# Optimization experiments

Hardware: AMD Instinct MI355X
Metric: run time of the kernel (lower is better)

Reference implementation:

```python
import jax, jax.numpy as jnp
import numpy as np

S, L, B = 64, 64, 16
D_IN, D_ATTN = 1024, 512


def setup_inputs() -> dict:
    key = jax.random.key(0)
    ks = jax.random.split(key, 8)
    context = jax.random.normal(ks[0], (S, L, B, D_IN), dtype=jnp.float32)
    query = jax.random.normal(ks[1], (L, B, D_IN), dtype=jnp.float32)
    mask = jnp.ones((S, L, B), dtype=jnp.int32)
    # Linear params (torch layout: weight [out, in], bias [out])
    sc = 1.0 / np.sqrt(D_IN)
    Wc = jax.random.uniform(ks[2], (D_ATTN, D_IN), minval=-sc, maxval=sc, dtype=jnp.float32)
    bc = jax.random.uniform(ks[3], (D_ATTN,), minval=-sc, maxval=sc, dtype=jnp.float32)
    Wq = jax.random.uniform(ks[4], (D_ATTN, D_IN), minval=-sc, maxval=sc, dtype=jnp.float32)
    bq = jax.random.uniform(ks[5], (D_ATTN,), minval=-sc, maxval=sc, dtype=jnp.float32)
    v = jax.random.uniform(ks[6], (D_ATTN,), dtype=jnp.float32)  # torch.rand -> U[0,1)
    return {"context": context, "query": query, "mask": mask,
            "Wc": Wc, "bc": bc, "Wq": Wq, "bq": bq, "v": v}


def reference(context, query, mask, Wc, bc, Wq, bq, v):
    # context: [s,l,b,din], query: [l,b,din]
    context_proj = jnp.einsum('slbi,di->slbd', context, Wc) + bc  # [s,l,b,da]
    query_proj = jnp.einsum('lbi,di->lbd', query, Wq) + bq        # [l,b,da]
    scores = jnp.tanh(context_proj + query_proj[None])            # [s,l,b,da]
    scores = jnp.einsum('slbd,d->slb', scores, v)                 # [s,l,b]
    scores = jnp.where(mask == 0, jnp.float32(-1e9), scores)
    alpha = jax.nn.softmax(scores, axis=0)                        # softmax over s
    attn_output = jnp.einsum('slb,slbd->lbd', alpha, context)     # [l,b,din]
    return (attn_output, alpha)
```

## Files before the change

kernel.cpp:

```cpp
#include <hip/hip_runtime.h>
#include <hip/hip_fp16.h>
#include <stdint.h>

#define S_DIM 64
#define L_DIM 64
#define B_DIM 16
#define LB    1024
#define DIN   1024
#define DA    512
#define M_TOT 65536

#define BM 64
#define BN 256
#define BK 64
#define NT (DIN / BK)

using f16x8 = __attribute__((ext_vector_type(8))) _Float16;
using f32x4 = __attribute__((ext_vector_type(4))) float;

typedef const __attribute__((address_space(1))) void* gas_ptr;
typedef __attribute__((address_space(3))) void* las_ptr;

__device__ __forceinline__ void load_lds16(const void* g, void* l) {
    __builtin_amdgcn_global_load_lds((gas_ptr)g, (las_ptr)l, 16, 0, 0);
}

__device__ __forceinline__ float fast_tanh(float x) {
    return 1.0f - 2.0f / (__expf(2.0f * x) + 1.0f);
}

__global__ void cvt_all(const float* __restrict__ Wc, const float* __restrict__ Wq,
                        const float* __restrict__ q,
                        _Float16* __restrict__ Wch, _Float16* __restrict__ Wqh,
                        _Float16* __restrict__ Qh) {
    int i = blockIdx.x * 256 + threadIdx.x;
    if (i < DA * DIN)            Wch[i] = (_Float16)Wc[i];
    else if (i < 2 * DA * DIN)   Wqh[i - DA * DIN] = (_Float16)Wq[i - DA * DIN];
    else                         Qh[i - 2 * DA * DIN] = (_Float16)q[i - 2 * DA * DIN];
}

__global__ __launch_bounds__(256) void qp_gemm(
    const _Float16* __restrict__ Qh,
    const _Float16* __restrict__ Wqh,
    const float* __restrict__ bq, const float* __restrict__ bc,
    float* __restrict__ qp)
{
    __shared__ __align__(16) _Float16 lA[64 * 64];
    __shared__ __align__(16) _Float16 lB[64 * 64];
    const int t = threadIdx.x;
    const int w = t >> 6, lane = t & 63;
    const int quad = lane >> 4, m16 = lane & 15;
    const int n0 = blockIdx.x * 64, lb0 = blockIdx.y * 64;

    f32x4 acc[4] = {};

    for (int kt = 0; kt < DIN / 64; ++kt) {
#pragma unroll
        for (int i = 0; i < 2; ++i) {
            int c = (w * 2 + i) * 64 + lane;
            int row = c >> 3;
            int kc = (c & 7) ^ (row & 7);
            load_lds16(Qh  + (size_t)(lb0 + row) * DIN + kt * 64 + kc * 8, (char*)lA + (size_t)c * 16);
            load_lds16(Wqh + (size_t)(n0  + row) * DIN + kt * 64 + kc * 8, (char*)lB + (size_t)c * 16);
        }
        __syncthreads();
#pragma unroll
        for (int kk = 0; kk < 64; kk += 32) {
            int cq = (kk >> 3) + quad;
            int ar = 16 * w + m16;
            f16x8 a = *(const f16x8*)((const char*)lA + ar * 128 + ((cq ^ (ar & 7)) * 16));
#pragma unroll
            for (int j = 0; j < 4; ++j) {
                int br = 16 * j + m16;
                f16x8 b = *(const f16x8*)((const char*)lB + br * 128 + ((cq ^ (br & 7)) * 16));
                acc[j] = __builtin_amdgcn_mfma_f32_16x16x32_f16(a, b, acc[j], 0, 0, 0);
            }
        }
        __syncthreads();
    }
#pragma unroll
    for (int j = 0; j < 4; ++j) {
        int n = n0 + 16 * j + m16;
        float bias = bq[n] + bc[n];
#pragma unroll
        for (int r = 0; r < 4; ++r) {
            int lb = lb0 + 16 * w + quad * 4 + r;
            qp[(size_t)lb * DA + n] = acc[j][r] + bias;
        }
    }
}

__global__ __launch_bounds__(256, 3) void score_gemm6(
    const float* __restrict__ ctx,
    const _Float16* __restrict__ Wch,
    const float* __restrict__ qp,
    const float* __restrict__ v,
    _Float16* __restrict__ ctxh,
    float* __restrict__ sc)
{
    __shared__ __align__(16) _Float16 lA[BM * BK];
    __shared__ __align__(16) _Float16 lB[BN * BK];
    __shared__ float lP[4][BM];

    const int t = threadIdx.x;
    const int w = t >> 6, lane = t & 63;
    const int quad = lane >> 4, m16 = lane & 15;
    const int wn = w;

    int bid = blockIdx.x;
    int xcd = bid & 7;
    int idx = bid >> 3;
    const int nq = idx & 1;
    const int mb = xcd * 128 + (idx >> 1);
    const int m0 = mb * BM;
    const int n0 = nq * BN;
    const int lb0 = m0 & (LB - 1);
    const bool wr_ctxh = (nq == 0);

    const int arow = t >> 2;
    const int c0   = (t & 3) * 2;

    auto stageB = [&](int kt) {
#pragma unroll
        for (int i = 0; i < 8; ++i) {
            int c = (w * 8 + i) * 64 + lane;
            int row = c >> 3;
            int kc = (c & 7) ^ (row & 7);
            load_lds16(Wch + (size_t)(n0 + row) * DIN + kt * BK + kc * 8,
                       (char*)lB + (size_t)c * 16);
        }
    };

    f32x4 pf[4];
    auto issueA = [&](int kt) {
        const float* p = ctx + (size_t)(m0 + arow) * DIN + kt * BK + c0 * 8;
        pf[0] = *(const f32x4*)(p);
        pf[1] = *(const f32x4*)(p + 4);
        pf[2] = *(const f32x4*)(p + 8);
        pf[3] = *(const f32x4*)(p + 12);
    };

    issueA(0);

    f32x4 acc[4][4];
#pragma unroll
    for (int i = 0; i < 4; ++i) {
        int rl = lb0 + 16 * i + quad * 4;
#pragma unroll
        for (int j = 0; j < 4; ++j) {
            int n = n0 + wn * 64 + 16 * j + m16;
#pragma unroll
            for (int r = 0; r < 4; ++r)
                acc[i][j][r] = qp[(size_t)(rl + r) * DA + n];
        }
    }

    for (int kt = 0; kt < NT; ++kt) {
        stageB(kt);

        f16x8 h0 = {(_Float16)pf[0][0], (_Float16)pf[0][1], (_Float16)pf[0][2], (_Float16)pf[0][3],
                    (_Float16)pf[1][0], (_Float16)pf[1][1], (_Float16)pf[1][2], (_Float16)pf[1][3]};
        f16x8 h1 = {(_Float16)pf[2][0], (_Float16)pf[2][1], (_Float16)pf[2][2], (_Float16)pf[2][3],
                    (_Float16)pf[3][0], (_Float16)pf[3][1], (_Float16)pf[3][2], (_Float16)pf[3][3]};
        *(f16x8*)((char*)lA + arow * 128 + (((c0)     ^ (arow & 7)) * 16)) = h0;
        *(f16x8*)((char*)lA + arow * 128 + (((c0 + 1) ^ (arow & 7)) * 16)) = h1;
        if (wr_ctxh) {
            _Float16* cd = ctxh + (size_t)(m0 + arow) * DIN + kt * BK + c0 * 8;
            *(f16x8*)cd = h0;
            *(f16x8*)(cd + 8) = h1;
        }

        issueA(kt + 1 < NT ? kt + 1 : NT - 1);

        if (wr_ctxh) asm volatile("s_waitcnt vmcnt(6)" ::: "memory");
        else         asm volatile("s_waitcnt vmcnt(4)" ::: "memory");
        asm volatile("s_waitcnt lgkmcnt(0)" ::: "memory");
        __builtin_amdgcn_s_barrier();
        __builtin_amdgcn_sched_barrier(0);

#pragma unroll
        for (int kk2 = 0; kk2 < 2; ++kk2) {
            int cq = kk2 * 4 + quad;
            f16x8 a[4], b[4];
#pragma unroll
            for (int i = 0; i < 4; ++i) {
                int ar = 16 * i + m16;
                a[i] = *(const f16x8*)((const char*)lA + ar * 128 + ((cq ^ (ar & 7)) * 16));
            }
#pragma unroll
            for (int j = 0; j < 4; ++j) {
                int br = wn * 64 + 16 * j + m16;
                b[j] = *(const f16x8*)((const char*)lB + br * 128 + ((cq ^ (br & 7)) * 16));
            }
            __builtin_amdgcn_s_setprio(1);
#pragma unroll
            for (int i = 0; i < 4; ++i)
#pragma unroll
                for (int j = 0; j < 4; ++j)
                    acc[i][j] = __builtin_amdgcn_mfma_f32_16x16x32_f16(a[i], b[j], acc[i][j], 0, 0, 0);
            __builtin_amdgcn_s_setprio(0);
        }

        __builtin_amdgcn_sched_barrier(0);
        __builtin_amdgcn_s_barrier();
        __builtin_amdgcn_sched_barrier(0);
    }

    float vv[4];
#pragma unroll
    for (int j = 0; j < 4; ++j) vv[j] = v[n0 + wn * 64 + 16 * j + m16];

    float part[16];
#pragma unroll
    for (int i = 0; i < 4; ++i)
#pragma unroll
        for (int r = 0; r < 4; ++r) {
            float s = 0.f;
#pragma unroll
            for (int j = 0; j < 4; ++j)
                s += fast_tanh(acc[i][j][r]) * vv[j];
            part[i * 4 + r] = s;
        }
#pragma unroll
    for (int off = 1; off < 16; off <<= 1) {
#pragma unroll
        for (int k = 0; k < 16; ++k) part[k] += __shfl_xor(part[k], off, 64);
    }
    if (m16 == 0) {
#pragma unroll
        for (int k = 0; k < 16; ++k) {
            int rl = 16 * (k >> 2) + quad * 4 + (k & 3);
            lP[wn][rl] = part[k];
        }
    }
    __syncthreads();
    if (t < BM) {
        float s = lP[0][t] + lP[1][t] + lP[2][t] + lP[3][t];
        sc[(size_t)nq * M_TOT + m0 + t] = s;
    }
}

__global__ __launch_bounds__(256, 3) void score_gemm(
    const float* __restrict__ ctx, const _Float16* __restrict__ Wch,
    const float* __restrict__ qp, const float* __restrict__ v,
    float* __restrict__ scores)
{
    __shared__ __align__(16) _Float16 lA[128 * 64];
    __shared__ __align__(16) _Float16 lB[128 * 64];
    __shared__ float lP[2][128];

    const int t = threadIdx.x;
    const int w = t >> 6, lane = t & 63;
    const int quad = lane >> 4, m16 = lane & 15;
    const int wm = w & 1, wn = w >> 1;

    int bid = blockIdx.x;
    int xcd = bid & 7;
    int j2 = bid >> 3;
    int nqf = j2 & 3;
    int mbf = ((j2 >> 2) << 3) | xcd;
    const int m0 = mbf * 128;
    const int n0 = nqf * 128;

    f32x4 acc[4][4] = {};

    const int arow = t >> 1;
    const int akc4 = (t & 1) * 4;
    const float* gA = ctx + (size_t)(m0 + arow) * DIN + (t & 1) * 32;

    for (int kt = 0; kt < DIN / 64; ++kt) {
        {
            const float* p = gA + kt * 64;
            f32x4 f[8];
#pragma unroll
            for (int qd = 0; qd < 8; ++qd) f[qd] = *(const f32x4*)(p + qd * 4);
#pragma unroll
            for (int q2 = 0; q2 < 4; ++q2) {
                f16x8 h = {(_Float16)f[2*q2][0], (_Float16)f[2*q2][1],
                           (_Float16)f[2*q2][2], (_Float16)f[2*q2][3],
                           (_Float16)f[2*q2+1][0], (_Float16)f[2*q2+1][1],
                           (_Float16)f[2*q2+1][2], (_Float16)f[2*q2+1][3]};
                int c = akc4 + q2;
                *(f16x8*)((char*)lA + arow * 128 + ((c ^ (arow & 7)) * 16)) = h;
            }
        }
#pragma unroll
        for (int i = 0; i < 4; ++i) {
            int c = (w * 4 + i) * 64 + lane;
            int row = c >> 3;
            int kc = (c & 7) ^ (row & 7);
            load_lds16(Wch + (size_t)(n0 + row) * DIN + kt * 64 + kc * 8, (char*)lB + (size_t)c * 16);
        }
        __syncthreads();
#pragma unroll
        for (int kk = 0; kk < 64; kk += 32) {
            int cq = (kk >> 3) + quad;
            f16x8 a[4], b[4];
#pragma unroll
            for (int i = 0; i < 4; ++i) {
                int ar = wm * 64 + 16 * i + m16;
                a[i] = *(const f16x8*)((const char*)lA + ar * 128 + ((cq ^ (ar & 7)) * 16));
            }
#pragma unroll
            for (int j = 0; j < 4; ++j) {
                int br = wn * 64 + 16 * j + m16;
                b[j] = *(const f16x8*)((const char*)lB + br * 128 + ((cq ^ (br & 7)) * 16));
            }
#pragma unroll
            for (int i = 0; i < 4; ++i)
#pragma unroll
                for (int j = 0; j < 4; ++j)
                    acc[i][j] = __builtin_amdgcn_mfma_f32_16x16x32_f16(a[i], b[j], acc[i][j], 0, 0, 0);
        }
        __syncthreads();
    }

    float vv[4];
    int nn[4];
#pragma unroll
    for (int j = 0; j < 4; ++j) { nn[j] = n0 + wn * 64 + 16 * j + m16; vv[j] = v[nn[j]]; }

    float part[16];
#pragma unroll
    for (int i = 0; i < 4; ++i) {
#pragma unroll
        for (int r = 0; r < 4; ++r) {
            int gm = m0 + wm * 64 + 16 * i + quad * 4 + r;
            int lb = gm & (LB - 1);
            float s = 0.f;
#pragma unroll
            for (int j = 0; j < 4; ++j) {
                float x = acc[i][j][r] + qp[(size_t)lb * DA + nn[j]];
                s += fast_tanh(x) * vv[j];
            }
            part[i * 4 + r] = s;
        }
    }
#pragma unroll
    for (int off = 1; off < 16; off <<= 1) {
#pragma unroll
        for (int k = 0; k < 16; ++k) part[k] += __shfl_xor(part[k], off, 64);
    }
    if (m16 == 0) {
#pragma unroll
        for (int k = 0; k < 16; ++k) {
            int row_local = wm * 64 + 16 * (k >> 2) + quad * 4 + (k & 3);
            lP[wn][row_local] = part[k];
        }
    }
    __syncthreads();
    if (t < 128) {
        float s = lP[0][t] + lP[1][t];
        atomicAdd(&scores[m0 + t], s);
    }
}

__global__ __launch_bounds__(64) void softmax3(const float* __restrict__ sc,
                                               const int* __restrict__ mask,
                                               float* __restrict__ alpha) {
    int lb = blockIdx.x;
    int s = threadIdx.x;
    int m = s * LB + lb;
    float x = sc[m] + sc[M_TOT + m];
    if (mask[m] == 0) x = -1e9f;
    float mx = x;
#pragma unroll
    for (int off = 1; off < 64; off <<= 1) mx = fmaxf(mx, __shfl_xor(mx, off, 64));
    float e = __expf(x - mx);
    float sum = e;
#pragma unroll
    for (int off = 1; off < 64; off <<= 1) sum += __shfl_xor(sum, off, 64);
    alpha[m] = e / sum;
}

__global__ __launch_bounds__(64) void softmax2(const float* __restrict__ scores,
                                               const int* __restrict__ mask,
                                               float* __restrict__ alpha) {
    int lb = blockIdx.x;
    int s = threadIdx.x;
    float x = scores[s * LB + lb];
    if (mask[s * LB + lb] == 0) x = -1e9f;
    float mx = x;
#pragma unroll
    for (int off = 1; off < 64; off <<= 1) mx = fmaxf(mx, __shfl_xor(mx, off, 64));
    float e = __expf(x - mx);
    float sum = e;
#pragma unroll
    for (int off = 1; off < 64; off <<= 1) sum += __shfl_xor(sum, off, 64);
    alpha[s * LB + lb] = e / sum;
}

__global__ __launch_bounds__(128) void weighted_sum2(
    const _Float16* __restrict__ ctxh, const float* __restrict__ alpha,
    float* __restrict__ out) {
    __shared__ float lAl[S_DIM];
    const int lb = blockIdx.x;
    const int t = threadIdx.x;
    if (t < S_DIM) lAl[t] = alpha[t * LB + lb];
    __syncthreads();
    float acc[8] = {};
    const _Float16* base = ctxh + (size_t)lb * DIN + t * 8;
#pragma unroll 8
    for (int s = 0; s < S_DIM; ++s) {
        float a = lAl[s];
        f16x8 c = *(const f16x8*)(base + (size_t)s * LB * DIN);
#pragma unroll
        for (int j = 0; j < 8; ++j) acc[j] += a * (float)c[j];
    }
    f32x4 lo = {acc[0], acc[1], acc[2], acc[3]};
    f32x4 hi = {acc[4], acc[5], acc[6], acc[7]};
    *(f32x4*)(out + (size_t)lb * DIN + t * 8) = lo;
    *(f32x4*)(out + (size_t)lb * DIN + t * 8 + 4) = hi;
}

__global__ __launch_bounds__(256) void weighted_sum(
    const float* __restrict__ ctx, const float* __restrict__ alpha,
    float* __restrict__ out) {
    __shared__ float lAl[S_DIM];
    const int lb = blockIdx.x;
    const int t = threadIdx.x;
    if (t < S_DIM) lAl[t] = alpha[t * LB + lb];
    __syncthreads();
    f32x4 acc = {0.f, 0.f, 0.f, 0.f};
    const float* base = ctx + (size_t)lb * DIN + t * 4;
#pragma unroll 4
    for (int s = 0; s < S_DIM; ++s) {
        float a = lAl[s];
        f32x4 c = *(const f32x4*)(base + (size_t)s * LB * DIN);
        acc += a * c;
    }
    *(f32x4*)(out + (size_t)lb * DIN + t * 4) = acc;
}

extern "C" void kernel_launch(void* const* d_in, const int* in_sizes, int n_in,
                              void* d_out, int out_size, void* d_ws, size_t ws_size,
                              hipStream_t stream) {
    (void)in_sizes; (void)n_in; (void)out_size;
    const float* ctx   = (const float*)d_in[0];
    const float* query = (const float*)d_in[1];
    const int*   mask  = (const int*)d_in[2];
    const float* Wc    = (const float*)d_in[3];
    const float* bc    = (const float*)d_in[4];
    const float* Wq    = (const float*)d_in[5];
    const float* bq    = (const float*)d_in[6];
    const float* v     = (const float*)d_in[7];

    float* out_attn  = (float*)d_out;
    float* out_alpha = (float*)d_out + (size_t)LB * DIN;

    char* ws = (char*)d_ws;
    _Float16* Wch = (_Float16*)(ws);
    _Float16* Wqh = (_Float16*)(ws + (1 << 20));
    _Float16* Qh  = (_Float16*)(ws + (2 << 20));
    float*    qp  = (float*)(ws + (4 << 20));
    float*    sc  = (float*)(ws + (6 << 20));
    _Float16* ctxh = (_Float16*)(ws + (8 << 20));

    const size_t need = (size_t)(8 + 128) << 20;
    const bool bigws = ws_size >= need;

    cvt_all<<<(2 * DA * DIN + LB * DIN) / 256, 256, 0, stream>>>(Wc, Wq, query, Wch, Wqh, Qh);
    qp_gemm<<<dim3(DA / 64, LB / 64), 256, 0, stream>>>(Qh, Wqh, bq, bc, qp);

    if (bigws) {
        score_gemm6<<<(M_TOT / BM) * (DA / BN), 256, 0, stream>>>(ctx, Wch, qp, v, ctxh, sc);
        softmax3<<<LB, 64, 0, stream>>>(sc, mask, out_alpha);
        weighted_sum2<<<LB, 128, 0, stream>>>(ctxh, out_alpha, out_attn);
    } else {
        hipMemsetAsync(sc, 0, (size_t)M_TOT * sizeof(float), stream);
        score_gemm<<<2048, 256, 0, stream>>>(ctx, Wch, qp, v, sc);
        softmax2<<<LB, 64, 0, stream>>>(sc, mask, out_alpha);
        weighted_sum<<<LB, 256, 0, stream>>>(ctx, out_alpha, out_attn);
    }
}
```

Measured before the change: 496.7 us.

## Double-buffer score GEMM LDS, halve N tile, split weighted sum over s

The score GEMM now uses double-buffered LDS for the A and B tiles. The next k-tile is converted and staged while the current one feeds the MFMAs, and the trailing barrier per iteration is gone. The N tile shrinks from 256 to 128, so four blocks per M tile each write partial scores, and softmax now sums four partial score planes. The weighted sum kernel uses 512 threads, splitting the s loop four ways and reducing through shared memory to raise parallelism. The trade-off is that context is re-read and converted by four blocks per M tile instead of two, adding global traffic.

```diff
diff --git a/kernel.cpp b/kernel.cpp
--- a/kernel.cpp
+++ b/kernel.cpp
@@ -11,7 +11,7 @@
 #define M_TOT 65536
 
 #define BM 64
-#define BN 256
+#define BN 128
 #define BK 64
 #define NT (DIN / BK)
 
@@ -90,7 +90,7 @@
     }
 }
 
-__global__ __launch_bounds__(256, 3) void score_gemm6(
+__global__ __launch_bounds__(256, 3) void score_gemm7(
     const float* __restrict__ ctx,
     const _Float16* __restrict__ Wch,
     const float* __restrict__ qp,
@@ -98,8 +98,8 @@
     _Float16* __restrict__ ctxh,
     float* __restrict__ sc)
 {
-    __shared__ __align__(16) _Float16 lA[BM * BK];
-    __shared__ __align__(16) _Float16 lB[BN * BK];
+    __shared__ __align__(16) _Float16 lA[2][BM * BK];
+    __shared__ __align__(16) _Float16 lB[2][BN * BK];
     __shared__ float lP[4][BM];
 
     const int t = threadIdx.x;
@@ -110,8 +110,8 @@
     int bid = blockIdx.x;
     int xcd = bid & 7;
     int idx = bid >> 3;
-    const int nq = idx & 1;
-    const int mb = xcd * 128 + (idx >> 1);
+    const int nq = idx & 3;
+    const int mb = xcd * 128 + (idx >> 2);
     const int m0 = mb * BM;
     const int n0 = nq * BN;
     const int lb0 = m0 & (LB - 1);
@@ -120,14 +120,14 @@
     const int arow = t >> 2;
     const int c0   = (t & 3) * 2;
 
-    auto stageB = [&](int kt) {
-#pragma unroll
-        for (int i = 0; i < 8; ++i) {
-            int c = (w * 8 + i) * 64 + lane;
+    auto stageB = [&](int kt, int buf) {
+#pragma unroll
+        for (int i = 0; i < 4; ++i) {
+            int c = (w * 4 + i) * 64 + lane;
             int row = c >> 3;
             int kc = (c & 7) ^ (row & 7);
             load_lds16(Wch + (size_t)(n0 + row) * DIN + kt * BK + kc * 8,
-                       (char*)lB + (size_t)c * 16);
+                       (char*)lB[buf] + (size_t)c * 16);
         }
     };
 
@@ -140,75 +140,83 @@
         pf[3] = *(const f32x4*)(p + 12);
     };
 
-    issueA(0);
-
-    f32x4 acc[4][4];
-#pragma unroll
-    for (int i = 0; i < 4; ++i) {
-        int rl = lb0 + 16 * i + quad * 4;
-#pragma unroll
-        for (int j = 0; j < 4; ++j) {
-            int n = n0 + wn * 64 + 16 * j + m16;
-#pragma unroll
-            for (int r = 0; r < 4; ++r)
-                acc[i][j][r] = qp[(size_t)(rl + r) * DA + n];
-        }
-    }
-
-    for (int kt = 0; kt < NT; ++kt) {
-        stageB(kt);
-
+    auto cvtStore = [&](int kts) {
         f16x8 h0 = {(_Float16)pf[0][0], (_Float16)pf[0][1], (_Float16)pf[0][2], (_Float16)pf[0][3],
                     (_Float16)pf[1][0], (_Float16)pf[1][1], (_Float16)pf[1][2], (_Float16)pf[1][3]};
         f16x8 h1 = {(_Float16)pf[2][0], (_Float16)pf[2][1], (_Float16)pf[2][2], (_Float16)pf[2][3],
                     (_Float16)pf[3][0], (_Float16)pf[3][1], (_Float16)pf[3][2], (_Float16)pf[3][3]};
-        *(f16x8*)((char*)lA + arow * 128 + (((c0)     ^ (arow & 7)) * 16)) = h0;
-        *(f16x8*)((char*)lA + arow * 128 + (((c0 + 1) ^ (arow & 7)) * 16)) = h1;
+        char* base = (char*)lA[kts & 1];
+        *(f16x8*)(base + arow * 128 + (((c0)     ^ (arow & 7)) * 16)) = h0;
+        *(f16x8*)(base + arow * 128 + (((c0 + 1) ^ (arow & 7)) * 16)) = h1;
         if (wr_ctxh) {
-            _Float16* cd = ctxh + (size_t)(m0 + arow) * DIN + kt * BK + c0 * 8;
+            _Float16* cd = ctxh + (size_t)(m0 + arow) * DIN + kts * BK + c0 * 8;
             *(f16x8*)cd = h0;
             *(f16x8*)(cd + 8) = h1;
         }
-
-        issueA(kt + 1 < NT ? kt + 1 : NT - 1);
-
-        if (wr_ctxh) asm volatile("s_waitcnt vmcnt(6)" ::: "memory");
-        else         asm volatile("s_waitcnt vmcnt(4)" ::: "memory");
+    };
+
+    issueA(0);
+
+    f32x4 acc[4][2];
+#pragma unroll
+    for (int i = 0; i < 4; ++i) {
+        int rl = lb0 + 16 * i + quad * 4;
+#pragma unroll
+        for (int j = 0; j < 2; ++j) {
+            int n = n0 + wn * 32 + 16 * j + m16;
+#pragma unroll
+            for (int r = 0; r < 4; ++r)
+                acc[i][j][r] = qp[(size_t)(rl + r) * DA + n];
+        }
+    }
+
+    cvtStore(0);
+    stageB(0, 0);
+    issueA(1);
+
+    for (int kt = 0; kt < NT; ++kt) {
+        const int cur = kt & 1;
+
+        if (kt == NT - 1) asm volatile("s_waitcnt vmcnt(0)" ::: "memory");
+        else              asm volatile("s_waitcnt vmcnt(4)" ::: "memory");
         asm volatile("s_waitcnt lgkmcnt(0)" ::: "memory");
         __builtin_amdgcn_s_barrier();
         __builtin_amdgcn_sched_barrier(0);
 
+        if (kt + 1 < NT) {
+            cvtStore(kt + 1);
+            stageB(kt + 1, cur ^ 1);
+            if (kt + 2 < NT) issueA(kt + 2);
+        }
+        __builtin_amdgcn_sched_barrier(0);
+
 #pragma unroll
         for (int kk2 = 0; kk2 < 2; ++kk2) {
             int cq = kk2 * 4 + quad;
-            f16x8 a[4], b[4];
+            f16x8 a[4], b[2];
 #pragma unroll
             for (int i = 0; i < 4; ++i) {
                 int ar = 16 * i + m16;
-                a[i] = *(const f16x8*)((const char*)lA + ar * 128 + ((cq ^ (ar & 7)) * 16));
-            }
-#pragma unroll
-            for (int j = 0; j < 4; ++j) {
-                int br = wn * 64 + 16 * j + m16;
-                b[j] = *(const f16x8*)((const char*)lB + br * 128 + ((cq ^ (br & 7)) * 16));
+                a[i] = *(const f16x8*)((const char*)lA[cur] + ar * 128 + ((cq ^ (ar & 7)) * 16));
+            }
+#pragma unroll
+            for (int j = 0; j < 2; ++j) {
+                int br = wn * 32 + 16 * j + m16;
+                b[j] = *(const f16x8*)((const char*)lB[cur] + br * 128 + ((cq ^ (br & 7)) * 16));
             }
             __builtin_amdgcn_s_setprio(1);
 #pragma unroll
             for (int i = 0; i < 4; ++i)
 #pragma unroll
-                for (int j = 0; j < 4; ++j)
+                for (int j = 0; j < 2; ++j)
                     acc[i][j] = __builtin_amdgcn_mfma_f32_16x16x32_f16(a[i], b[j], acc[i][j], 0, 0, 0);
             __builtin_amdgcn_s_setprio(0);
         }
-
-        __builtin_amdgcn_sched_barrier(0);
-        __builtin_amdgcn_s_barrier();
-        __builtin_amdgcn_sched_barrier(0);
-    }
-
-    float vv[4];
-#pragma unroll
-    for (int j = 0; j < 4; ++j) vv[j] = v[n0 + wn * 64 + 16 * j + m16];
+    }
+
+    float vv[2];
+#pragma unroll
+    for (int j = 0; j < 2; ++j) vv[j] = v[n0 + wn * 32 + 16 * j + m16];
 
     float part[16];
 #pragma unroll
@@ -217,7 +225,7 @@
         for (int r = 0; r < 4; ++r) {
             float s = 0.f;
 #pragma unroll
-            for (int j = 0; j < 4; ++j)
+            for (int j = 0; j < 2; ++j)
                 s += fast_tanh(acc[i][j][r]) * vv[j];
             part[i * 4 + r] = s;
         }
@@ -355,13 +363,13 @@
     }
 }
 
-__global__ __launch_bounds__(64) void softmax3(const float* __restrict__ sc,
+__global__ __launch_bounds__(64) void softmax4(const float* __restrict__ sc,
                                                const int* __restrict__ mask,
                                                float* __restrict__ alpha) {
     int lb = blockIdx.x;
     int s = threadIdx.x;
     int m = s * LB + lb;
-    float x = sc[m] + sc[M_TOT + m];
+    float x = sc[m] + sc[M_TOT + m] + sc[2 * M_TOT + m] + sc[3 * M_TOT + m];
     if (mask[m] == 0) x = -1e9f;
     float mx = x;
 #pragma unroll
@@ -390,27 +398,41 @@
     alpha[s * LB + lb] = e / sum;
 }
 
-__global__ __launch_bounds__(128) void weighted_sum2(
+__global__ __launch_bounds__(512) void weighted_sum3(
     const _Float16* __restrict__ ctxh, const float* __restrict__ alpha,
     float* __restrict__ out) {
     __shared__ float lAl[S_DIM];
+    __shared__ float red[4][DIN];
     const int lb = blockIdx.x;
     const int t = threadIdx.x;
     if (t < S_DIM) lAl[t] = alpha[t * LB + lb];
     __syncthreads();
+    const int d8 = t & 127;
+    const int sq = t >> 7;
     float acc[8] = {};
-    const _Float16* base = ctxh + (size_t)lb * DIN + t * 8;
-#pragma unroll 8
-    for (int s = 0; s < S_DIM; ++s) {
+    const _Float16* base = ctxh + (size_t)lb * DIN + d8 * 8;
+#pragma unroll 4
+    for (int s = sq * 16; s < sq * 16 + 16; ++s) {
         float a = lAl[s];
         f16x8 c = *(const f16x8*)(base + (size_t)s * LB * DIN);
 #pragma unroll
         for (int j = 0; j < 8; ++j) acc[j] += a * (float)c[j];
     }
-    f32x4 lo = {acc[0], acc[1], acc[2], acc[3]};
-    f32x4 hi = {acc[4], acc[5], acc[6], acc[7]};
-    *(f32x4*)(out + (size_t)lb * DIN + t * 8) = lo;
-    *(f32x4*)(out + (size_t)lb * DIN + t * 8 + 4) = hi;
+#pragma unroll
+    for (int j = 0; j < 8; ++j) red[sq][d8 * 8 + j] = acc[j];
+    __syncthreads();
+    if (t < 128) {
+        float o[8];
+#pragma unroll
+        for (int j = 0; j < 8; ++j) {
+            int d = t * 8 + j;
+            o[j] = red[0][d] + red[1][d] + red[2][d] + red[3][d];
+        }
+        f32x4 lo = {o[0], o[1], o[2], o[3]};
+        f32x4 hi = {o[4], o[5], o[6], o[7]};
+        *(f32x4*)(out + (size_t)lb * DIN + t * 8) = lo;
+        *(f32x4*)(out + (size_t)lb * DIN + t * 8 + 4) = hi;
+    }
 }
 
 __global__ __launch_bounds__(256) void weighted_sum(
@@ -463,9 +485,9 @@
     qp_gemm<<<dim3(DA / 64, LB / 64), 256, 0, stream>>>(Qh, Wqh, bq, bc, qp);
 
     if (bigws) {
-        score_gemm6<<<(M_TOT / BM) * (DA / BN), 256, 0, stream>>>(ctx, Wch, qp, v, ctxh, sc);
-        softmax3<<<LB, 64, 0, stream>>>(sc, mask, out_alpha);
-        weighted_sum2<<<LB, 128, 0, stream>>>(ctxh, out_alpha, out_attn);
+        score_gemm7<<<(M_TOT / BM) * (DA / BN), 256, 0, stream>>>(ctx, Wch, qp, v, ctxh, sc);
+        softmax4<<<LB, 64, 0, stream>>>(sc, mask, out_alpha);
+        weighted_sum3<<<LB, 512, 0, stream>>>(ctxh, out_alpha, out_attn);
     } else {
         hipMemsetAsync(sc, 0, (size_t)M_TOT * sizeof(float), stream);
         score_gemm<<<2048, 256, 0, stream>>>(ctx, Wch, qp, v, sc);
```

Measured after the change: 528.9 us. 1.06x slower.
